# Kernel optimization log

Measured on AMD Instinct MI355X. Metric: run time of the kernel, lower is better.

Reference implementation:

```python
import jax, jax.numpy as jnp
import numpy as np

NEG_SLOPE = 0.2  # PyG GATv2Conv default negative_slope


def _gatv2(h, src, dst, Wl, bl, Wr, br, att, bias, N):
    """GATv2Conv (concat=True). h: [N,Fin]; att: [H,F]; returns [N,H*F]."""
    H, F = att.shape
    xl = (h @ Wl + bl).reshape(N, H, F)  # source transform
    xr = (h @ Wr + br).reshape(N, H, F)  # target transform
    # per-edge GATv2 score: a^T LeakyReLU(xl[src] + xr[dst])
    e = jax.nn.leaky_relu(xl[src] + xr[dst], negative_slope=NEG_SLOPE)  # [E,H,F]
    logits = jnp.einsum('ehf,hf->eh', e, att)  # [E,H]
    # segment softmax over destination nodes (self-loops guarantee nonempty segments)
    m = jax.ops.segment_max(logits, dst, num_segments=N)  # [N,H]
    p = jnp.exp(logits - m[dst])
    s = jax.ops.segment_sum(p, dst, num_segments=N)  # [N,H]
    alpha = p / s[dst]  # [E,H]
    out = jax.ops.segment_sum(alpha[:, :, None] * xl[src], dst, num_segments=N)  # [N,H,F]
    return out.reshape(N, H * F) + bias


def setup_inputs() -> dict:
    key = jax.random.key(0)
    ks = jax.random.split(key, 16)
    N, E = 30000, 480000
    L, D, H, F = 50, 100, 3, 100
    W = D * H  # 300
    sc = 0.1  # keep activations stable through 5 layers
    return {
        'x': jax.random.randint(ks[0], (N,), 0, L),
        'edge_index': jax.random.randint(ks[1], (2, E), 0, N),
        'emb': jax.random.normal(ks[2], (L, D), jnp.float32),
        'Wl0': jax.random.normal(ks[3], (D, W), jnp.float32) * sc,
        'bl0': jnp.zeros((W,), jnp.float32),
        'Wr0': jax.random.normal(ks[4], (D, W), jnp.float32) * sc,
        'br0': jnp.zeros((W,), jnp.float32),
        'att0': jax.random.normal(ks[5], (H, F), jnp.float32) * sc,
        'bias0': jnp.zeros((W,), jnp.float32),
        'Wl': jax.random.normal(ks[6], (4, W, W), jnp.float32) * sc,
        'bl': jnp.zeros((4, W), jnp.float32),
        'Wr': jax.random.normal(ks[7], (4, W, W), jnp.float32) * sc,
        'br': jnp.zeros((4, W), jnp.float32),
        'att': jax.random.normal(ks[8], (4, H, F), jnp.float32) * sc,
        'bias': jnp.zeros((4, W), jnp.float32),
    }


def reference(x, edge_index, emb, Wl0, bl0, Wr0, br0, att0, bias0,
              Wl, bl, Wr, br, att, bias):
    N = x.shape[0]
    loops = jnp.arange(N)
    src = jnp.concatenate([edge_index[0], loops])  # PyG add_self_loops=True
    dst = jnp.concatenate([edge_index[1], loops])
    h = emb[x]  # node_embedding(x).squeeze()
    h = jax.nn.relu(_gatv2(h, src, dst, Wl0, bl0, Wr0, br0, att0, bias0, N))
    for i in range(4):  # remaining num_gnn_layers-1 convs, each followed by ReLU
        h = jax.nn.relu(_gatv2(h, src, dst, Wl[i], bl[i], Wr[i], br[i], att[i], bias[i], N))
    return h  # [N, heads*hidden] = [N, 300]
```

## Files before the change

kernel.cpp:

```cpp
#include <hip/hip_runtime.h>

#define NODES   30000
#define E0N     480000
#define ETOT    510000
#define D0      100
#define WDIM    300
#define NW      600
#define NEG     0.2f
#define XLP     384

typedef __bf16 bf16x8 __attribute__((ext_vector_type(8)));
typedef float  f32x4  __attribute__((ext_vector_type(4)));
typedef float  f32x2  __attribute__((ext_vector_type(2)));
#define BCAST2(x) ((f32x2){(x), (x)})

__global__ void count_edges(const int* __restrict__ ei, int* __restrict__ counts) {
    int e = blockIdx.x * 256 + threadIdx.x;
    if (e >= ETOT) return;
    int d = (e < E0N) ? ei[E0N + e] : (e - E0N);
    atomicAdd(&counts[d], 1);
}

__global__ __launch_bounds__(1024) void scan_kernel(const int* __restrict__ counts,
                                                    int* __restrict__ offsets, int n) {
    __shared__ int lds[1024];
    const int CH = 32;
    int t = threadIdx.x;
    int base = t * CH;
    int loc[CH];
    int sum = 0;
    #pragma unroll
    for (int i = 0; i < CH; i++) {
        int v = (base + i < n) ? counts[base + i] : 0;
        loc[i] = sum;
        sum += v;
    }
    lds[t] = sum;
    __syncthreads();
    for (int off = 1; off < 1024; off <<= 1) {
        int v = (t >= off) ? lds[t - off] : 0;
        __syncthreads();
        lds[t] += v;
        __syncthreads();
    }
    int ex = (t == 0) ? 0 : lds[t - 1];
    #pragma unroll
    for (int i = 0; i < CH; i++) {
        int idx = base + i;
        if (idx < n) offsets[idx] = ex + loc[i];
    }
    if (t == 0) offsets[n] = lds[1023];
}

__global__ void scatter_edges(const int* __restrict__ ei, const int* __restrict__ offsets,
                              int* __restrict__ cursor, int* __restrict__ csr_off) {
    int e = blockIdx.x * 256 + threadIdx.x;
    if (e >= ETOT) return;
    int s, d;
    if (e < E0N) { s = ei[e]; d = ei[E0N + e]; }
    else         { s = e - E0N; d = s; }
    int pos = offsets[d] + atomicAdd(&cursor[d], 1);
    csr_off[pos] = s * XLP;
}

__device__ __forceinline__ void bfrag_one(const float* Bl, const float* Br,
                                          bf16x8* out, int K, int t) {
    int lane = t & 63;
    int n16  = (t >> 6) % 40;
    int s    = t / (64 * 40);
    int c = n16 * 16 + (lane & 15);
    union { bf16x8 v; __bf16 e[8]; } hi, lo;
    #pragma unroll
    for (int j = 0; j < 8; j++) {
        int k = s * 32 + ((lane >> 4) * 8) + j;
        float x = 0.f;
        if (k < K && c < NW)
            x = (c < WDIM) ? Bl[(size_t)k * WDIM + c] : Br[(size_t)k * WDIM + c - WDIM];
        __bf16 h = (__bf16)x;
        hi.e[j] = h;
        lo.e[j] = (__bf16)(x - (float)h);
    }
    size_t base = ((size_t)(s * 40 + n16) * 2) * 64 + lane;
    out[base]      = hi.v;
    out[base + 64] = lo.v;
}

__global__ void make_bfrag_all(const float* __restrict__ Wl0, const float* __restrict__ Wr0,
                               const float* __restrict__ Wl, const float* __restrict__ Wr,
                               bf16x8* __restrict__ frag0, bf16x8* __restrict__ frag1,
                               size_t fragstride) {
    int t = blockIdx.x * 256 + threadIdx.x;
    const int L0 = 4 * 40 * 64, LN = 10 * 40 * 64;
    if (t < L0) {
        bfrag_one(Wl0, Wr0, frag0, D0, t);
    } else {
        int u = t - L0;
        int layer = u / LN;
        if (layer >= 4) return;
        bfrag_one(Wl + (size_t)layer * WDIM * WDIM, Wr + (size_t)layer * WDIM * WDIM,
                  frag1 + layer * fragstride, WDIM, u - layer * LN);
    }
}

__global__ __launch_bounds__(256) void gemm_mfma(
    const float* __restrict__ A, const int* __restrict__ xmap, int use_map,
    const bf16x8* __restrict__ Bfrag,
    const float* __restrict__ bl, const float* __restrict__ br,
    ushort* __restrict__ Cl16, float* __restrict__ Cr,
    int M, int K, int ksteps) {

    __shared__ bf16x8 Alds[8][2][64];

    int id = blockIdx.x;
    int mb = (id & 7) + 8 * (id / 40);
    int cb = (id >> 3) % 5;
    if (mb >= 235) return;

    int tid  = threadIdx.x;
    int lane = tid & 63;
    int wid  = tid >> 6;
    int wm = wid >> 1, wn = wid & 1;
    int row0 = mb * 128;

    f32x4 acc[4][4] = {};

    for (int s = 0; s < ksteps; s++) {
        int kt = s * 32;
        #pragma unroll
        for (int u0 = 0; u0 < 2; u0++) {
            int u = u0 * 256 + tid;
            int m16  = u >> 6;
            int slot = u & 63;
            int kh = slot >> 4, rl = slot & 15;
            int gr = row0 + m16 * 16 + rl;
            int gc = kt + kh * 8;
            float4 v0 = make_float4(0.f,0.f,0.f,0.f), v1 = v0;
            if (gr < M) {
                int ar = use_map ? xmap[gr] : gr;
                const float* ap = A + (size_t)ar * K + gc;
                if (gc + 4 <= K) v0 = *(const float4*)ap;
                if (gc + 8 <= K) v1 = *(const float4*)(ap + 4);
            }
            union { bf16x8 v; __bf16 e[8]; } hi, lo;
            const float* xs0 = (const float*)&v0;
            const float* xs1 = (const float*)&v1;
            #pragma unroll
            for (int j = 0; j < 8; j++) {
                float x = (j < 4) ? xs0[j] : xs1[j - 4];
                __bf16 h = (__bf16)x;
                hi.e[j] = h;
                lo.e[j] = (__bf16)(x - (float)h);
            }
            Alds[m16][0][slot] = hi.v;
            Alds[m16][1][slot] = lo.v;
        }
        bf16x8 bfr[4][2];
        {
            const bf16x8* bwave = Bfrag + ((size_t)(s * 40 + cb * 8 + wn * 4) * 2) * 64;
            #pragma unroll
            for (int n = 0; n < 4; n++) {
                bfr[n][0] = bwave[(n * 2 + 0) * 64 + lane];
                bfr[n][1] = bwave[(n * 2 + 1) * 64 + lane];
            }
        }
        __syncthreads();

        bf16x8 af[4][2];
        #pragma unroll
        for (int m = 0; m < 4; m++) {
            af[m][0] = Alds[wm * 4 + m][0][lane];
            af[m][1] = Alds[wm * 4 + m][1][lane];
        }
        #pragma unroll
        for (int m = 0; m < 4; m++)
            #pragma unroll
            for (int n = 0; n < 4; n++) {
                acc[m][n] = __builtin_amdgcn_mfma_f32_16x16x32_bf16(af[m][1], bfr[n][0], acc[m][n], 0, 0, 0);
                acc[m][n] = __builtin_amdgcn_mfma_f32_16x16x32_bf16(af[m][0], bfr[n][1], acc[m][n], 0, 0, 0);
                acc[m][n] = __builtin_amdgcn_mfma_f32_16x16x32_bf16(af[m][0], bfr[n][0], acc[m][n], 0, 0, 0);
            }
        __syncthreads();
    }

    int r0 = row0 + wm * 64;
    int c0 = cb * 128 + wn * 64;
    #pragma unroll
    for (int m = 0; m < 4; m++)
        #pragma unroll
        for (int n = 0; n < 4; n++) {
            #pragma unroll
            for (int reg = 0; reg < 4; reg++) {
                int gr = r0 + m * 16 + (lane >> 4) * 4 + reg;
                int gc = c0 + n * 16 + (lane & 15);
                if (gr < M && gc < NW) {
                    if (gc < WDIM) {
                        float v = acc[m][n][reg] + bl[gc];
                        int head = gc / 100;
                        int fh = gc - head * 100;
                        __bf16 b = (__bf16)v;
                        Cl16[(size_t)gr * XLP + head * 128 + fh] = *(ushort*)&b;
                    } else {
                        int cc = gc - WDIM;
                        Cr[(size_t)gr * WDIM + cc] = acc[m][n][reg] + br[cc];
                    }
                }
            }
        }
}

__device__ __forceinline__ f32x2 bf2f2(unsigned u) {
    f32x2 r;
    r.x = __uint_as_float(u << 16);
    r.y = __uint_as_float(u & 0xffff0000u);
    return r;
}
__device__ __forceinline__ f32x2 lrelu2(f32x2 t) {
    return __builtin_elementwise_max(t, t * BCAST2(NEG));
}

__global__ __launch_bounds__(256) void gat_edge_agg(
    const ushort* __restrict__ xl, const float* __restrict__ xr,
    const int* __restrict__ offsets, const int* __restrict__ csr_off,
    const float* __restrict__ att, const float* __restrict__ bias,
    float* __restrict__ fout) {
    __shared__ float st[4][64][10];
    int wid  = threadIdx.x >> 6;
    int lane = threadIdx.x & 63;
    int node = blockIdx.x * 2 + (wid >> 1);
    int sub  = wid & 1;
    int lq    = lane & 31;
    int headq = lane >> 5;

    f32x2 aw4[2] = {}, xr4[2] = {}, awp = {}, xrp = {};
    if (lq < 25) {
        float4 a = *(const float4*)(att + headq * 100 + 4 * lq);
        float4 b = *(const float4*)(xr + (size_t)node * WDIM + headq * 100 + 4 * lq);
        aw4[0] = (f32x2){a.x, a.y}; aw4[1] = (f32x2){a.z, a.w};
        xr4[0] = (f32x2){b.x, b.y}; xr4[1] = (f32x2){b.z, b.w};
    }
    if (lane < 50) {
        float2 a = *(const float2*)(att + 200 + 2 * lane);
        float2 b = *(const float2*)(xr + (size_t)node * WDIM + 200 + 2 * lane);
        awp = (f32x2){a.x, a.y};
        xrp = (f32x2){b.x, b.y};
    }

    float m_h = -1e38f, s_h = 0.f, m_2 = -1e38f, s_2 = 0.f;
    f32x2 acc4[2] = {}, accp = {};

    int beg = offsets[node], end = offsets[node + 1];
    int half = (end - beg + 1) >> 1;
    int lo = beg + sub * half;
    int iend = sub ? end : beg + half;

    for (int i = lo; i < iend; i += 2) {
        bool act_b = (i + 1) < iend;
        int oa = csr_off[i];
        int ob = csr_off[act_b ? i + 1 : i];
        uint2 ua = *(const uint2*)(xl + oa + 4 * lane);
        uint2 ub = *(const uint2*)(xl + ob + 4 * lane);
        unsigned pa = *(const unsigned*)(xl + oa + 256 + 2 * lane);
        unsigned pb = *(const unsigned*)(xl + ob + 256 + 2 * lane);

        f32x2 va0 = bf2f2(ua.x), va1 = bf2f2(ua.y), vap = bf2f2(pa);
        f32x2 vb0 = bf2f2(ub.x), vb1 = bf2f2(ub.y), vbp = bf2f2(pb);

        f32x2 tA = __builtin_elementwise_fma(lrelu2(va0 + xr4[0]), aw4[0],
                                             lrelu2(va1 + xr4[1]) * aw4[1]);
        f32x2 tB = __builtin_elementwise_fma(lrelu2(vb0 + xr4[0]), aw4[0],
                                             lrelu2(vb1 + xr4[1]) * aw4[1]);
        f32x2 tA2 = lrelu2(vap + xrp) * awp;
        f32x2 tB2 = lrelu2(vbp + xrp) * awp;
        float qA  = tA.x + tA.y,   qB  = tB.x + tB.y;
        float qA2 = tA2.x + tA2.y, qB2 = tB2.x + tB2.y;

        qA += __shfl_xor(qA, 1, 64);  qB += __shfl_xor(qB, 1, 64);
        qA += __shfl_xor(qA, 2, 64);  qB += __shfl_xor(qB, 2, 64);
        qA += __shfl_xor(qA, 4, 64);  qB += __shfl_xor(qB, 4, 64);
        qA += __shfl_xor(qA, 8, 64);  qB += __shfl_xor(qB, 8, 64);
        qA += __shfl_xor(qA, 16, 64); qB += __shfl_xor(qB, 16, 64);
        qA2 += __shfl_xor(qA2, 1, 64);  qB2 += __shfl_xor(qB2, 1, 64);
        qA2 += __shfl_xor(qA2, 2, 64);  qB2 += __shfl_xor(qB2, 2, 64);
        qA2 += __shfl_xor(qA2, 4, 64);  qB2 += __shfl_xor(qB2, 4, 64);
        qA2 += __shfl_xor(qA2, 8, 64);  qB2 += __shfl_xor(qB2, 8, 64);
        qA2 += __shfl_xor(qA2, 16, 64); qB2 += __shfl_xor(qB2, 16, 64);
        qA2 += __shfl_xor(qA2, 32, 64); qB2 += __shfl_xor(qB2, 32, 64);
        if (!act_b) { qB = -3e38f; qB2 = -3e38f; }

        float hi_h = fmaxf(qA, qB), hi_2 = fmaxf(qA2, qB2);
        if (__any(hi_h > m_h + 8.f || hi_2 > m_2 + 8.f)) {
            float nm_h = fmaxf(m_h, hi_h), nm_2 = fmaxf(m_2, hi_2);
            float e_h = __expf(m_h - nm_h), e_2 = __expf(m_2 - nm_2);
            s_h *= e_h; s_2 *= e_2;
            acc4[0] *= BCAST2(e_h); acc4[1] *= BCAST2(e_h);
            accp *= BCAST2(e_2);
            m_h = nm_h; m_2 = nm_2;
        }
        float cA  = __expf(qA - m_h),  cB  = __expf(qB - m_h);
        float cA2 = __expf(qA2 - m_2), cB2 = __expf(qB2 - m_2);
        s_h += cA + cB; s_2 += cA2 + cB2;
        acc4[0] = __builtin_elementwise_fma(BCAST2(cA), va0, acc4[0]);
        acc4[1] = __builtin_elementwise_fma(BCAST2(cA), va1, acc4[1]);
        acc4[0] = __builtin_elementwise_fma(BCAST2(cB), vb0, acc4[0]);
        acc4[1] = __builtin_elementwise_fma(BCAST2(cB), vb1, acc4[1]);
        accp    = __builtin_elementwise_fma(BCAST2(cA2), vap, accp);
        accp    = __builtin_elementwise_fma(BCAST2(cB2), vbp, accp);
    }

    st[wid][lane][0] = m_h; st[wid][lane][1] = s_h;
    st[wid][lane][2] = m_2; st[wid][lane][3] = s_2;
    st[wid][lane][4] = acc4[0].x; st[wid][lane][5] = acc4[0].y;
    st[wid][lane][6] = acc4[1].x; st[wid][lane][7] = acc4[1].y;
    st[wid][lane][8] = accp.x;    st[wid][lane][9] = accp.y;
    __syncthreads();
    if (sub) return;

    const float* p = st[wid ^ 1][lane];
    float pm_h = p[0], ps_h = p[1], pm_2 = p[2], ps_2 = p[3];

    float M_h = fmaxf(m_h, pm_h);
    float ea_h = __expf(m_h - M_h), eb_h = __expf(pm_h - M_h);
    float inv_h = 1.f / (s_h * ea_h + ps_h * eb_h);
    float M_2 = fmaxf(m_2, pm_2);
    float ea_2 = __expf(m_2 - M_2), eb_2 = __expf(pm_2 - M_2);
    float inv_2 = 1.f / (s_2 * ea_2 + ps_2 * eb_2);

    if (lq < 25) {
        float4 bv = *(const float4*)(bias + headq * 100 + 4 * lq);
        float4 o;
        o.x = fmaxf((acc4[0].x * ea_h + p[4] * eb_h) * inv_h + bv.x, 0.f);
        o.y = fmaxf((acc4[0].y * ea_h + p[5] * eb_h) * inv_h + bv.y, 0.f);
        o.z = fmaxf((acc4[1].x * ea_h + p[6] * eb_h) * inv_h + bv.z, 0.f);
        o.w = fmaxf((acc4[1].y * ea_h + p[7] * eb_h) * inv_h + bv.w, 0.f);
        *(float4*)(fout + (size_t)node * WDIM + headq * 100 + 4 * lq) = o;
    }
    if (lane < 50) {
        float2 bv = *(const float2*)(bias + 200 + 2 * lane);
        float2 o;
        o.x = fmaxf((accp.x * ea_2 + p[8] * eb_2) * inv_2 + bv.x, 0.f);
        o.y = fmaxf((accp.y * ea_2 + p[9] * eb_2) * inv_2 + bv.y, 0.f);
        *(float2*)(fout + (size_t)node * WDIM + 200 + 2 * lane) = o;
    }
}

static inline size_t align256(size_t x) { return (x + 255) & ~(size_t)255; }

extern "C" void kernel_launch(void* const* d_in, const int* in_sizes, int n_in,
                              void* d_out, int out_size, void* d_ws, size_t ws_size,
                              hipStream_t stream) {
    const int*   x     = (const int*)d_in[0];
    const int*   ei    = (const int*)d_in[1];
    const float* emb   = (const float*)d_in[2];
    const float* Wl0   = (const float*)d_in[3];
    const float* bl0   = (const float*)d_in[4];
    const float* Wr0   = (const float*)d_in[5];
    const float* br0   = (const float*)d_in[6];
    const float* att0  = (const float*)d_in[7];
    const float* bias0 = (const float*)d_in[8];
    const float* Wl    = (const float*)d_in[9];
    const float* bl    = (const float*)d_in[10];
    const float* Wr    = (const float*)d_in[11];
    const float* br    = (const float*)d_in[12];
    const float* att   = (const float*)d_in[13];
    const float* bias  = (const float*)d_in[14];

    char* ws = (char*)d_ws;
    size_t off = 0;
    float* h      = (float*)(ws + off);  off = align256(off + (size_t)NODES * WDIM * 4);
    ushort* xlb16 = (ushort*)(ws + off); off = align256(off + (size_t)NODES * XLP * 2);
    float* xrb    = (float*)(ws + off);  off = align256(off + (size_t)NODES * WDIM * 4);
    int* counts   = (int*)(ws + off);    off = align256(off + (size_t)NODES * 4);
    int* cursor   = (int*)(ws + off);    off = align256(off + (size_t)NODES * 4);
    int* offsets  = (int*)(ws + off);    off = align256(off + (size_t)(NODES + 1) * 4);
    int* csr_off  = (int*)(ws + off);    off = align256(off + (size_t)ETOT * 4);
    size_t frag_l0_elems = (size_t)4 * 40 * 2 * 64;
    size_t frag_ln_elems = (size_t)10 * 40 * 2 * 64;
    bf16x8* bfrag0 = (bf16x8*)(ws + off); off = align256(off + frag_l0_elems * 16);
    bf16x8* bfrag1 = (bf16x8*)(ws + off); off = align256(off + 4 * frag_ln_elems * 16);

    float* out = (float*)d_out;

    {
        int total = 4 * 40 * 64 + 4 * 10 * 40 * 64;
        make_bfrag_all<<<(total + 255) / 256, 256, 0, stream>>>(
            Wl0, Wr0, Wl, Wr, bfrag0, bfrag1, frag_ln_elems);
    }

    hipMemsetAsync(counts, 0, (size_t)NODES * 4, stream);
    hipMemsetAsync(cursor, 0, (size_t)NODES * 4, stream);
    count_edges<<<(ETOT + 255) / 256, 256, 0, stream>>>(ei, counts);
    scan_kernel<<<1, 1024, 0, stream>>>(counts, offsets, NODES);
    scatter_edges<<<(ETOT + 255) / 256, 256, 0, stream>>>(ei, offsets, cursor, csr_off);

    int agg_blocks = NODES / 2;

    gemm_mfma<<<1200, 256, 0, stream>>>(emb, x, 1, bfrag0, bl0, br0, xlb16, xrb, NODES, D0, 4);
    gat_edge_agg<<<agg_blocks, 256, 0, stream>>>(xlb16, xrb, offsets, csr_off, att0, bias0, h);

    for (int i = 0; i < 4; i++) {
        float* dst = (i == 3) ? out : h;
        gemm_mfma<<<1200, 256, 0, stream>>>(h, nullptr, 0, bfrag1 + i * frag_ln_elems,
                                            bl + i * WDIM, br + i * WDIM,
                                            xlb16, xrb, NODES, WDIM, 10);
        gat_edge_agg<<<agg_blocks, 256, 0, stream>>>(xlb16, xrb, offsets, csr_off,
                                                     att + (size_t)i * WDIM,
                                                     bias + (size_t)i * WDIM, dst);
    }
}
```

Measured before the change: 813.4 us.

## Sort nodes by degree for aggregation, cheaper bf16 split, merged shuffle reductions

Adds a degree histogram and counting sort so that aggregation blocks process nodes in descending-degree order. This is meant to reduce load imbalance and tail effects in the per-node edge loop. It also replaces the round-to-nearest bf16 hi/lo split with a truncation-based bit split in the GEMM and weight packing, and packs the two edges' logit reductions into one shuffle chain using lane parity, which halves the exp count. The cost is extra setup kernels, an indirection load per block, and slightly different rounding in the split-bf16 GEMM.

```diff
diff --git a/kernel.cpp b/kernel.cpp
--- a/kernel.cpp
+++ b/kernel.cpp
@@ -8,6 +8,7 @@
 #define NW      600
 #define NEG     0.2f
 #define XLP     384
+#define NBIN    1024
 
 typedef __bf16 bf16x8 __attribute__((ext_vector_type(8)));
 typedef float  f32x4  __attribute__((ext_vector_type(4)));
@@ -63,26 +64,77 @@
     csr_off[pos] = s * XLP;
 }
 
+__global__ void hist_deg(const int* __restrict__ counts, int* __restrict__ hist) {
+    __shared__ int lh[NBIN];
+    for (int i = threadIdx.x; i < NBIN; i += 256) lh[i] = 0;
+    __syncthreads();
+    int n = blockIdx.x * 256 + threadIdx.x;
+    if (n < NODES) {
+        int d = counts[n]; if (d > NBIN - 1) d = NBIN - 1;
+        atomicAdd(&lh[NBIN - 1 - d], 1);
+    }
+    __syncthreads();
+    for (int i = threadIdx.x; i < NBIN; i += 256) {
+        int v = lh[i];
+        if (v) atomicAdd(&hist[i], v);
+    }
+}
+
+__global__ void scatter_deg(const int* __restrict__ counts, const int* __restrict__ doffs,
+                            int* __restrict__ dcur, int* __restrict__ order) {
+    __shared__ int lcnt[NBIN];
+    __shared__ int lbase[NBIN];
+    for (int i = threadIdx.x; i < NBIN; i += 256) lcnt[i] = 0;
+    __syncthreads();
+    int n = blockIdx.x * 256 + threadIdx.x;
+    int bin = 0, rank = 0;
+    bool act = n < NODES;
+    if (act) {
+        int d = counts[n]; if (d > NBIN - 1) d = NBIN - 1;
+        bin = NBIN - 1 - d;
+        rank = atomicAdd(&lcnt[bin], 1);
+    }
+    __syncthreads();
+    for (int i = threadIdx.x; i < NBIN; i += 256) {
+        int c = lcnt[i];
+        lbase[i] = c ? atomicAdd(&dcur[i], c) : 0;
+    }
+    __syncthreads();
+    if (act) order[doffs[bin] + lbase[bin] + rank] = n;
+}
+
+__device__ __forceinline__ void trunc_split2(float a, float b,
+                                             unsigned& hp, unsigned& lp) {
+    unsigned ua = __float_as_uint(a), ub = __float_as_uint(b);
+    hp = (ua >> 16) | (ub & 0xffff0000u);
+    float la = a - __uint_as_float(ua & 0xffff0000u);
+    float lb = b - __uint_as_float(ub & 0xffff0000u);
+    lp = (__float_as_uint(la) >> 16) | (__float_as_uint(lb) & 0xffff0000u);
+}
+
 __device__ __forceinline__ void bfrag_one(const float* Bl, const float* Br,
                                           bf16x8* out, int K, int t) {
     int lane = t & 63;
     int n16  = (t >> 6) % 40;
     int s    = t / (64 * 40);
     int c = n16 * 16 + (lane & 15);
-    union { bf16x8 v; __bf16 e[8]; } hi, lo;
+    float x[8];
     #pragma unroll
     for (int j = 0; j < 8; j++) {
         int k = s * 32 + ((lane >> 4) * 8) + j;
-        float x = 0.f;
+        float v = 0.f;
         if (k < K && c < NW)
-            x = (c < WDIM) ? Bl[(size_t)k * WDIM + c] : Br[(size_t)k * WDIM + c - WDIM];
-        __bf16 h = (__bf16)x;
-        hi.e[j] = h;
-        lo.e[j] = (__bf16)(x - (float)h);
-    }
+            v = (c < WDIM) ? Bl[(size_t)k * WDIM + c] : Br[(size_t)k * WDIM + c - WDIM];
+        x[j] = v;
+    }
+    uint4 hp, lp;
+    trunc_split2(x[0], x[1], hp.x, lp.x);
+    trunc_split2(x[2], x[3], hp.y, lp.y);
+    trunc_split2(x[4], x[5], hp.z, lp.z);
+    trunc_split2(x[6], x[7], hp.w, lp.w);
     size_t base = ((size_t)(s * 40 + n16) * 2) * 64 + lane;
-    out[base]      = hi.v;
-    out[base + 64] = lo.v;
+    *(uint4*)&out[base]      = hp;
+    *(uint4*)&out[base + 64] = lp;
 }
 
 __global__ void make_bfrag_all(const float* __restrict__ Wl0, const float* __restrict__ Wr0,
@@ -141,18 +193,13 @@
                 if (gc + 4 <= K) v0 = *(const float4*)ap;
                 if (gc + 8 <= K) v1 = *(const float4*)(ap + 4);
             }
-            union { bf16x8 v; __bf16 e[8]; } hi, lo;
-            const float* xs0 = (const float*)&v0;
-            const float* xs1 = (const float*)&v1;
-            #pragma unroll
-            for (int j = 0; j < 8; j++) {
-                float x = (j < 4) ? xs0[j] : xs1[j - 4];
-                __bf16 h = (__bf16)x;
-                hi.e[j] = h;
-                lo.e[j] = (__bf16)(x - (float)h);
-            }
-            Alds[m16][0][slot] = hi.v;
-            Alds[m16][1][slot] = lo.v;
+            uint4 hp, lp;
+            trunc_split2(v0.x, v0.y, hp.x, lp.x);
+            trunc_split2(v0.z, v0.w, hp.y, lp.y);
+            trunc_split2(v1.x, v1.y, hp.z, lp.z);
+            trunc_split2(v1.z, v1.w, hp.w, lp.w);
+            *(uint4*)&Alds[m16][0][slot] = hp;
+            *(uint4*)&Alds[m16][1][slot] = lp;
         }
         bf16x8 bfr[4][2];
         {
@@ -221,15 +268,17 @@
 __global__ __launch_bounds__(256) void gat_edge_agg(
     const ushort* __restrict__ xl, const float* __restrict__ xr,
     const int* __restrict__ offsets, const int* __restrict__ csr_off,
+    const int* __restrict__ order,
     const float* __restrict__ att, const float* __restrict__ bias,
     float* __restrict__ fout) {
     __shared__ float st[4][64][10];
     int wid  = threadIdx.x >> 6;
     int lane = threadIdx.x & 63;
-    int node = blockIdx.x * 2 + (wid >> 1);
+    int node = order[blockIdx.x * 2 + (wid >> 1)];
     int sub  = wid & 1;
     int lq    = lane & 31;
     int headq = lane >> 5;
+    int par   = lane & 1;
 
     f32x2 aw4[2] = {}, xr4[2] = {}, awp = {}, xrp = {};
     if (lq < 25) {
@@ -274,31 +323,40 @@
         float qA  = tA.x + tA.y,   qB  = tB.x + tB.y;
         float qA2 = tA2.x + tA2.y, qB2 = tB2.x + tB2.y;
 
-        qA += __shfl_xor(qA, 1, 64);  qB += __shfl_xor(qB, 1, 64);
-        qA += __shfl_xor(qA, 2, 64);  qB += __shfl_xor(qB, 2, 64);
-        qA += __shfl_xor(qA, 4, 64);  qB += __shfl_xor(qB, 4, 64);
-        qA += __shfl_xor(qA, 8, 64);  qB += __shfl_xor(qB, 8, 64);
-        qA += __shfl_xor(qA, 16, 64); qB += __shfl_xor(qB, 16, 64);
-        qA2 += __shfl_xor(qA2, 1, 64);  qB2 += __shfl_xor(qB2, 1, 64);
-        qA2 += __shfl_xor(qA2, 2, 64);  qB2 += __shfl_xor(qB2, 2, 64);
-        qA2 += __shfl_xor(qA2, 4, 64);  qB2 += __shfl_xor(qB2, 4, 64);
-        qA2 += __shfl_xor(qA2, 8, 64);  qB2 += __shfl_xor(qB2, 8, 64);
-        qA2 += __shfl_xor(qA2, 16, 64); qB2 += __shfl_xor(qB2, 16, 64);
-        qA2 += __shfl_xor(qA2, 32, 64); qB2 += __shfl_xor(qB2, 32, 64);
-        if (!act_b) { qB = -3e38f; qB2 = -3e38f; }
-
-        float hi_h = fmaxf(qA, qB), hi_2 = fmaxf(qA2, qB2);
-        if (__any(hi_h > m_h + 8.f || hi_2 > m_2 + 8.f)) {
-            float nm_h = fmaxf(m_h, hi_h), nm_2 = fmaxf(m_2, hi_2);
+        qA += __shfl_xor(qA, 1, 64);   qB += __shfl_xor(qB, 1, 64);
+        float u = par ? qB : qA;
+        u += __shfl_xor(u, 2, 64);
+        u += __shfl_xor(u, 4, 64);
+        u += __shfl_xor(u, 8, 64);
+        u += __shfl_xor(u, 16, 64);
+        qA2 += __shfl_xor(qA2, 1, 64); qB2 += __shfl_xor(qB2, 1, 64);
+        float v = par ? qB2 : qA2;
+        v += __shfl_xor(v, 2, 64);
+        v += __shfl_xor(v, 4, 64);
+        v += __shfl_xor(v, 8, 64);
+        v += __shfl_xor(v, 16, 64);
+        v += __shfl_xor(v, 32, 64);
+        if (!act_b && par) { u = -3e38f; v = -3e38f; }
+
+        float upair = fmaxf(u, __shfl_xor(u, 1, 64));
+        float vpair = fmaxf(v, __shfl_xor(v, 1, 64));
+
+        if (__any(upair > m_h + 8.f || vpair > m_2 + 8.f)) {
+            float nm_h = fmaxf(m_h, upair), nm_2 = fmaxf(m_2, vpair);
             float e_h = __expf(m_h - nm_h), e_2 = __expf(m_2 - nm_2);
             s_h *= e_h; s_2 *= e_2;
             acc4[0] *= BCAST2(e_h); acc4[1] *= BCAST2(e_h);
             accp *= BCAST2(e_2);
             m_h = nm_h; m_2 = nm_2;
         }
-        float cA  = __expf(qA - m_h),  cB  = __expf(qB - m_h);
-        float cA2 = __expf(qA2 - m_2), cB2 = __expf(qB2 - m_2);
-        s_h += cA + cB; s_2 += cA2 + cB2;
+        float cu = __expf(u - m_h);
+        float cv = __expf(v - m_2);
+        s_h += cu; s_2 += cv;
+        float cup = __shfl_xor(cu, 1, 64), cvp = __shfl_xor(cv, 1, 64);
+        float cA  = par ? cup : cu;
+        float cB  = par ? cu  : cup;
+        float cA2 = par ? cvp : cv;
+        float cB2 = par ? cv  : cvp;
         acc4[0] = __builtin_elementwise_fma(BCAST2(cA), va0, acc4[0]);
         acc4[1] = __builtin_elementwise_fma(BCAST2(cA), va1, acc4[1]);
         acc4[0] = __builtin_elementwise_fma(BCAST2(cB), vb0, acc4[0]);
@@ -306,6 +364,9 @@
         accp    = __builtin_elementwise_fma(BCAST2(cA2), vap, accp);
         accp    = __builtin_elementwise_fma(BCAST2(cB2), vbp, accp);
     }
+
+    s_h += __shfl_xor(s_h, 1, 64);
+    s_2 += __shfl_xor(s_2, 1, 64);
 
     st[wid][lane][0] = m_h; st[wid][lane][1] = s_h;
     st[wid][lane][2] = m_2; st[wid][lane][3] = s_2;
@@ -373,6 +434,10 @@
     int* cursor   = (int*)(ws + off);    off = align256(off + (size_t)NODES * 4);
     int* offsets  = (int*)(ws + off);    off = align256(off + (size_t)(NODES + 1) * 4);
     int* csr_off  = (int*)(ws + off);    off = align256(off + (size_t)ETOT * 4);
+    int* hist     = (int*)(ws + off);    off = align256(off + (size_t)NBIN * 4);
+    int* dcur     = (int*)(ws + off);    off = align256(off + (size_t)NBIN * 4);
+    int* doffs    = (int*)(ws + off);    off = align256(off + (size_t)(NBIN + 1) * 4);
+    int* order    = (int*)(ws + off);    off = align256(off + (size_t)NODES * 4);
     size_t frag_l0_elems = (size_t)4 * 40 * 2 * 64;
     size_t frag_ln_elems = (size_t)10 * 40 * 2 * 64;
     bf16x8* bfrag0 = (bf16x8*)(ws + off); off = align256(off + frag_l0_elems * 16);
@@ -388,21 +453,28 @@
 
     hipMemsetAsync(counts, 0, (size_t)NODES * 4, stream);
     hipMemsetAsync(cursor, 0, (size_t)NODES * 4, stream);
+    hipMemsetAsync(hist, 0, (size_t)NBIN * 4, stream);
+    hipMemsetAsync(dcur, 0, (size_t)NBIN * 4, stream);
     count_edges<<<(ETOT + 255) / 256, 256, 0, stream>>>(ei, counts);
     scan_kernel<<<1, 1024, 0, stream>>>(counts, offsets, NODES);
     scatter_edges<<<(ETOT + 255) / 256, 256, 0, stream>>>(ei, offsets, cursor, csr_off);
 
+    hist_deg<<<(NODES + 255) / 256, 256, 0, stream>>>(counts, hist);
+    scan_kernel<<<1, 1024, 0, stream>>>(hist, doffs, NBIN);
+    scatter_deg<<<(NODES + 255) / 256, 256, 0, stream>>>(counts, doffs, dcur, order);
+
     int agg_blocks = NODES / 2;
 
     gemm_mfma<<<1200, 256, 0, stream>>>(emb, x, 1, bfrag0, bl0, br0, xlb16, xrb, NODES, D0, 4);
-    gat_edge_agg<<<agg_blocks, 256, 0, stream>>>(xlb16, xrb, offsets, csr_off, att0, bias0, h);
+    gat_edge_agg<<<agg_blocks, 256, 0, stream>>>(xlb16, xrb, offsets, csr_off, order,
+                                                 att0, bias0, h);
 
     for (int i = 0; i < 4; i++) {
         float* dst = (i == 3) ? out : h;
         gemm_mfma<<<1200, 256, 0, stream>>>(h, nullptr, 0, bfrag1 + i * frag_ln_elems,
                                             bl + i * WDIM, br + i * WDIM,
                                             xlb16, xrb, NODES, WDIM, 10);
-        gat_edge_agg<<<agg_blocks, 256, 0, stream>>>(xlb16, xrb, offsets, csr_off,
+        gat_edge_agg<<<agg_blocks, 256, 0, stream>>>(xlb16, xrb, offsets, csr_off, order,
                                                      att + (size_t)i * WDIM,
                                                      bias + (size_t)i * WDIM, dst);
     }
```

Result: slower. 838.7 us (+3.1%).
